# Kernel optimization log

Measured on AMD Instinct MI355X. Metric: run time of the kernel, lower is better.

## Reference

```python
import jax, jax.numpy as jnp
import numpy as np

NEG_SLOPE = 0.01  # F.leaky_relu default
FGW = 0.1         # feature_guidance_weight


def gat_layer(x, src, dst, W, att_l, att_r, heads, out_ch, concat):
    N = x.shape[0]
    # reward-based guidance weights (L1-normalized over nodes, F.normalize p=1 dim=0)
    rw = 1.0 / (jnp.abs(x[:, -1:]) + 1e-6)                    # [N,1]
    rw = rw / jnp.maximum(jnp.sum(jnp.abs(rw), axis=0), 1e-12)
    h = (x @ W).reshape(N, heads, out_ch)                      # [N,H,C]
    # per-node attention halves, gathered per edge (avoids [E,H,C] for scores)
    al = jnp.sum(h * att_l, axis=-1)                           # [N,H] (x_i side)
    ar = jnp.sum(h * att_r, axis=-1)                           # [N,H] (x_j side)
    alpha = jax.nn.leaky_relu(al[dst] + ar[src], NEG_SLOPE)    # [E,H]
    alpha = alpha + FGW * jnp.log(rw[src])                     # guidance from source node
    # segment softmax over incoming edges of each target node (PyG softmax)
    m = jax.ops.segment_max(alpha, dst, num_segments=N)        # [N,H]
    e = jnp.exp(alpha - m[dst])
    s = jax.ops.segment_sum(e, dst, num_segments=N)
    alpha = e / (s[dst] + 1e-16)                               # [E,H]
    # weighted scatter-aggregate of source features
    msg = h[src] * alpha[:, :, None]                           # [E,H,C]
    out = jax.ops.segment_sum(msg, dst, num_segments=N)        # [N,H,C]
    if concat:
        return out.reshape(N, heads * out_ch)
    return out.mean(axis=1)


def setup_inputs() -> dict:
    key = jax.random.key(0)
    ks = jax.random.split(key, 10)
    N, E, D_IN, HID, HEADS, D_OUT = 50000, 800000, 128, 64, 4, 1

    def xavier(k, shape, fan_in, fan_out):
        a = jnp.sqrt(6.0 / (fan_in + fan_out))
        return jax.random.uniform(k, shape, jnp.float32, -a, a)

    x = jax.random.normal(ks[0], (N, D_IN), jnp.float32)
    edge_index = jax.random.randint(ks[1], (2, E), 0, N, jnp.int32)
    W1 = xavier(ks[2], (D_IN, HEADS * HID), D_IN, HEADS * HID)
    att_l1 = xavier(ks[3], (1, HEADS, HID), HID, HID)
    att_r1 = xavier(ks[4], (1, HEADS, HID), HID, HID)
    W2 = xavier(ks[5], (HEADS * HID, HID), HEADS * HID, HID)
    att_l2 = xavier(ks[6], (1, 1, HID), HID, HID)
    att_r2 = xavier(ks[7], (1, 1, HID), HID, HID)
    fc_w = xavier(ks[8], (HID, D_OUT), HID, D_OUT)
    fc_b = jnp.zeros((D_OUT,), jnp.float32)
    return {"x": x, "edge_index": edge_index, "W1": W1, "att_l1": att_l1,
            "att_r1": att_r1, "W2": W2, "att_l2": att_l2, "att_r2": att_r2,
            "fc_w": fc_w, "fc_b": fc_b}


def reference(x, edge_index, W1, att_l1, att_r1, W2, att_l2, att_r2, fc_w, fc_b):
    src, dst = edge_index[0], edge_index[1]
    HID, HEADS = 64, 4
    h = gat_layer(x, src, dst, W1, att_l1, att_r1, HEADS, HID, concat=True)
    h = jax.nn.elu(h)  # dropout omitted (eval mode)
    h = gat_layer(h, src, dst, W2, att_l2, att_r2, 1, HID, concat=False)
    h = jax.nn.elu(h)
    return h @ fc_w + fc_b
```

## Files before the change

kernel.cpp:

```cpp
#include <hip/hip_runtime.h>
#include <hip/hip_bf16.h>

typedef __hip_bfloat16 bf16;
typedef __attribute__((ext_vector_type(8))) short bf16x8;
typedef __attribute__((ext_vector_type(4))) float f32x4;

#define NEG_SLOPE 0.01f
#define FGW 0.1f

__device__ __forceinline__ float b2f(bf16 v) { return __bfloat162float(v); }

__device__ __forceinline__ float ldf(const void* p, size_t i, int isbf) {
    return isbf ? b2f(((const bf16*)p)[i]) : ((const float*)p)[i];
}

__device__ __forceinline__ float bu2f(unsigned short u) {
    return __uint_as_float(((unsigned)u) << 16);
}
__device__ __forceinline__ unsigned short f2bu(float f) {
    return __bfloat16_as_ushort(__float2bfloat16(f));
}

__device__ __forceinline__ float waveReduceSum(float v) {
#pragma unroll
    for (int o = 32; o > 0; o >>= 1) v += __shfl_down(v, o, 64);
    return v;
}

#define ATOMIC_ADD_F32(p, v) unsafeAtomicAdd((p), (v))

__global__ __launch_bounds__(256) void k_degdet(const int* __restrict__ ei, int* __restrict__ deg, int E,
                                                const unsigned short* __restrict__ xr,
                                                float* __restrict__ sscal, int* __restrict__ flag,
                                                const void* __restrict__ W1, const void* __restrict__ W2,
                                                unsigned short* __restrict__ Wp1h,
                                                unsigned short* __restrict__ Wp1l,
                                                unsigned short* __restrict__ Wp2) {
    __shared__ int sflag;
    const int t = threadIdx.x;
    const bool packer = (blockIdx.x < 128);
    if (packer) {
        if (t < 64) {
            int big = 0;
            for (int i = t; i < 256; i += 64) {
                int ex = (xr[i] >> 7) & 0xFF;
                if (ex >= 0xBF) big = 1;
            }
            unsigned long long mk = __ballot(big);
            if (t == 0) sflag = (mk == 0ull) ? 1 : 0;
        }
        __syncthreads();
        const int isbf = sflag;
        if (blockIdx.x == 0 && t == 0) {
            *flag = isbf;
            sscal[0] = 0.f; sscal[1] = 0.f;
        }
        int id = blockIdx.x * 256 + t;
        {
            int j = id & 7, l = (id >> 3) & 63, ko = (id >> 9) & 3, T = id >> 11;
            int k = ko * 32 + (l >> 4) * 8 + j, col = T * 16 + (l & 15);
            float wv = ldf(W1, (size_t)k * 256 + col, isbf);
            unsigned short hi = f2bu(wv);
            Wp1h[id] = hi;
            Wp1l[id] = f2bu(wv - bu2f(hi));
        }
        if (id < 16384) {
            int j = id & 7, l = (id >> 3) & 63, ko = (id >> 9) & 7, T = id >> 12;
            int k = ko * 32 + (l >> 4) * 8 + j, col = T * 16 + (l & 15);
            Wp2[id] = f2bu(ldf(W2, (size_t)k * 64 + col, isbf));
        }
    }
    int e = blockIdx.x * 256 + t;
    if (e < E) atomicAdd(&deg[ei[E + e]], 1);
}

__global__ __launch_bounds__(256) void k_scanA(const int* __restrict__ deg, int* __restrict__ tmp,
                                               int* __restrict__ bsum, int N) {
    __shared__ int part[256];
    const int t = threadIdx.x;
    int i = blockIdx.x * 256 + t;
    int v = (i < N) ? ((deg[i] + 3) & ~3) : 0;
    part[t] = v;
    __syncthreads();
    for (int o = 1; o < 256; o <<= 1) {
        int add = (t >= o) ? part[t - o] : 0;
        __syncthreads();
        part[t] += add;
        __syncthreads();
    }
    if (i < N) tmp[i] = part[t];
    if (t == 255) bsum[blockIdx.x] = part[255];
}

__global__ __launch_bounds__(256) void k_scanB(int* __restrict__ bsum, int nb, int* __restrict__ rowptrN) {
    __shared__ int part[256];
    const int t = threadIdx.x;
    const int K = (nb + 255) / 256;
    int vs[8];
    int lsum = 0;
#pragma unroll
    for (int k = 0; k < 8; k++) {
        int idx = t * K + k;
        vs[k] = (k < K && idx < nb) ? bsum[idx] : 0;
        lsum += vs[k];
    }
    part[t] = lsum;
    __syncthreads();
    for (int o = 1; o < 256; o <<= 1) {
        int add = (t >= o) ? part[t - o] : 0;
        __syncthreads();
        part[t] += add;
        __syncthreads();
    }
    int excl = part[t] - lsum;
#pragma unroll
    for (int k = 0; k < 8; k++) {
        int idx = t * K + k;
        if (k < K && idx < nb) { bsum[idx] = excl; excl += vs[k]; }
    }
    if (t == 255) *rowptrN = part[255];
}

__global__ __launch_bounds__(256) void k_scanC(const int* __restrict__ deg, const int* __restrict__ tmp,
                                               const int* __restrict__ bsum, int* __restrict__ rowptr,
                                               int* __restrict__ cursor, int* __restrict__ csr_src, int N) {
    int i = blockIdx.x * 256 + threadIdx.x;
    if (i >= N) return;
    int dg = deg[i];
    int pd = (dg + 3) & ~3;
    int base = bsum[blockIdx.x] + tmp[i] - pd;
    rowptr[i] = base;
    cursor[i] = 0;
    for (int j = dg; j < pd; j++) csr_src[base + j] = N;
}

__global__ __launch_bounds__(256) void k_scatter(const int* __restrict__ ei, const int* __restrict__ rowptr,
                                                 int* __restrict__ cursor, int* __restrict__ csr_src, int E) {
    int e = blockIdx.x * 256 + threadIdx.x;
    if (e >= E) return;
    int d = ei[E + e];
    int pos = atomicAdd(&cursor[d], 1);
    csr_src[rowptr[d] + pos] = ei[e];
}

__global__ __launch_bounds__(256) void k_gemm1f(const void* __restrict__ x,
                                                const unsigned short* __restrict__ Wp1h,
                                                const unsigned short* __restrict__ Wp1l,
                                                const void* __restrict__ attl,
                                                const void* __restrict__ attr,
                                                unsigned short* __restrict__ h1,
                                                float* __restrict__ pk1,
                                                float* __restrict__ al1,
                                                float* __restrict__ rwS,
                                                int N, const int* __restrict__ flag) {
    const int isbf = *flag;
    __shared__ unsigned short Ash[64 * 136];
    __shared__ unsigned short Asl[64 * 136];
    __shared__ float rpart[64];
    const int row0 = blockIdx.x * 64;
    const int t = threadIdx.x;
    const int w = t >> 6, lane = t & 63;
    const int m = lane & 15, quad = lane >> 4;

    if (blockIdx.x == 0) {
        if (t < 32) *reinterpret_cast<uint4*>(&h1[(size_t)N * 256 + t * 8]) = (uint4){0u, 0u, 0u, 0u};
        if (t < 8) pk1[(size_t)N * 8 + t] = (t < 4) ? -1e30f : 0.f;
    }

#pragma unroll
    for (int it = 0; it < 4; it++) {
        int idx = it * 256 + t;
        int r = idx >> 4, c = idx & 15;
        float v[8];
        if (row0 + r < N) {
            if (isbf) {
                const unsigned short* xu = (const unsigned short*)x;
                uint4 raw = *reinterpret_cast<const uint4*>(xu + (size_t)(row0 + r) * 128 + c * 8);
                const unsigned short* rs = (const unsigned short*)&raw;
#pragma unroll
                for (int k = 0; k < 8; k++) v[k] = bu2f(rs[k]);
            } else {
                const float* xf = (const float*)x;
                float4 a = *reinterpret_cast<const float4*>(xf + (size_t)(row0 + r) * 128 + c * 8);
                float4 b = *reinterpret_cast<const float4*>(xf + (size_t)(row0 + r) * 128 + c * 8 + 4);
                v[0] = a.x; v[1] = a.y; v[2] = a.z; v[3] = a.w;
                v[4] = b.x; v[5] = b.y; v[6] = b.z; v[7] = b.w;
            }
        } else {
#pragma unroll
            for (int k = 0; k < 8; k++) v[k] = 0.f;
        }
        unsigned short hi[8];
#pragma unroll
        for (int k = 0; k < 8; k++) hi[k] = f2bu(v[k]);
        *reinterpret_cast<uint4*>(&Ash[r * 136 + c * 8]) = *reinterpret_cast<const uint4*>(hi);
        if (!isbf) {
            unsigned short lo[8];
#pragma unroll
            for (int k = 0; k < 8; k++) lo[k] = f2bu(v[k] - bu2f(hi[k]));
            *reinterpret_cast<uint4*>(&Asl[r * 136 + c * 8]) = *reinterpret_cast<const uint4*>(lo);
        }
    }
    __syncthreads();

    bf16x8 Bh[4][4];
#pragma unroll
    for (int tt = 0; tt < 4; tt++)
#pragma unroll
        for (int ko = 0; ko < 4; ko++)
            Bh[tt][ko] = *reinterpret_cast<const bf16x8*>(
                &Wp1h[(size_t)(((w * 4 + tt) * 4 + ko) * 64 + lane) * 8]);
    float avl[4], avr[4];
#pragma unroll
    for (int tt = 0; tt < 4; tt++) {
        int col = (w * 4 + tt) * 16 + m;
        avl[tt] = ldf(attl, col, isbf);
        avr[tt] = ldf(attr, col, isbf);
    }
    for (int sub = 0; sub < 4; sub++) {
        const int rbase = sub * 16;
        bf16x8 Ah[4];
#pragma unroll
        for (int ko = 0; ko < 4; ko++)
            Ah[ko] = *reinterpret_cast<const bf16x8*>(&Ash[(rbase + m) * 136 + ko * 32 + quad * 8]);
        f32x4 Cf[4];
#pragma unroll
        for (int tt = 0; tt < 4; tt++) Cf[tt] = (f32x4){0.f, 0.f, 0.f, 0.f};
        if (isbf) {
#pragma unroll
            for (int ko = 0; ko < 4; ko++)
#pragma unroll
                for (int tt = 0; tt < 4; tt++)
                    Cf[tt] = __builtin_amdgcn_mfma_f32_16x16x32_bf16(Ah[ko], Bh[tt][ko], Cf[tt], 0, 0, 0);
        } else {
            bf16x8 Al[4];
#pragma unroll
            for (int ko = 0; ko < 4; ko++)
                Al[ko] = *reinterpret_cast<const bf16x8*>(&Asl[(rbase + m) * 136 + ko * 32 + quad * 8]);
#pragma unroll
            for (int ko = 0; ko < 4; ko++)
#pragma unroll
                for (int tt = 0; tt < 4; tt++) {
                    Cf[tt] = __builtin_amdgcn_mfma_f32_16x16x32_bf16(Ah[ko], Bh[tt][ko], Cf[tt], 0, 0, 0);
                    Cf[tt] = __builtin_amdgcn_mfma_f32_16x16x32_bf16(Al[ko], Bh[tt][ko], Cf[tt], 0, 0, 0);
                    bf16x8 Bl = *reinterpret_cast<const bf16x8*>(
                        &Wp1l[(size_t)(((w * 4 + tt) * 4 + ko) * 64 + lane) * 8]);
                    Cf[tt] = __builtin_amdgcn_mfma_f32_16x16x32_bf16(Ah[ko], Bl, Cf[tt], 0, 0, 0);
                }
        }
#pragma unroll
        for (int tt = 0; tt < 4; tt++) {
            int col = (w * 4 + tt) * 16 + m;
#pragma unroll
            for (int reg = 0; reg < 4; reg++) {
                int row = row0 + rbase + quad * 4 + reg;
                if (row < N) h1[(size_t)row * 256 + col] = f2bu(Cf[tt][reg]);
            }
        }
        if (w == 3 && m == 15) {
#pragma unroll
            for (int reg = 0; reg < 4; reg++) {
                int row = row0 + rbase + quad * 4 + reg;
                if (row < N) pk1[(size_t)row * 8 + 5] = Cf[3][reg];
            }
        }
        float sl[4], sr[4];
#pragma unroll
        for (int reg = 0; reg < 4; reg++) {
            float a = 0.f, b = 0.f;
#pragma unroll
            for (int tt = 0; tt < 4; tt++) {
                a = fmaf(avl[tt], Cf[tt][reg], a);
                b = fmaf(avr[tt], Cf[tt][reg], b);
            }
            sl[reg] = a; sr[reg] = b;
        }
#pragma unroll
        for (int off = 8; off >= 1; off >>= 1) {
#pragma unroll
            for (int reg = 0; reg < 4; reg++) {
                sl[reg] += __shfl_down(sl[reg], off, 64);
                sr[reg] += __shfl_down(sr[reg], off, 64);
            }
        }
        if (m == 0) {
#pragma unroll
            for (int reg = 0; reg < 4; reg++) {
                int row = row0 + rbase + quad * 4 + reg;
                if (row < N) {
                    al1[(size_t)row * 4 + w] = sl[reg];
                    pk1[(size_t)row * 8 + w] = sr[reg];
                }
            }
        }
    }
    if (t < 64) {
        int row = row0 + t;
        float rr = 0.f;
        if (row < N) {
            float a = fabsf(ldf(x, (size_t)row * 128 + 127, isbf));
            rr = 1.f / (a + 1e-6f);
            pk1[(size_t)row * 8 + 4] = logf(rr);
        }
        rpart[t] = rr;
    }
    __syncthreads();
    if (t == 0) {
        float s = 0.f;
#pragma unroll
        for (int i = 0; i < 64; i++) s += rpart[i];
        ATOMIC_ADD_F32(rwS, s);
    }
}

__global__ __launch_bounds__(256) void k_agg1(const int* __restrict__ rowptr,
                                              const int* __restrict__ csr_src,
                                              const float* __restrict__ al1,
                                              const float* __restrict__ pk1,
                                              const float* __restrict__ rwS,
                                              const unsigned short* __restrict__ h1,
                                              unsigned short* __restrict__ x2b,
                                              float* __restrict__ x2c, int N) {
    const int lane = threadIdx.x & 63;
    const int wid = threadIdx.x >> 6;
    const int q = lane & 15;
    const int g = lane >> 4;
    const int h = q >> 2;
    const bool last15 = (q == 15);
    const float gl = FGW * logf(fmaxf(*rwS, 1e-12f));
    const unsigned qo = (unsigned)q * 32u;
    const unsigned ho4 = (unsigned)h * 4u;
    const char* pk1c = (const char*)pk1;
    const char* h1c  = (const char*)h1;
    const int stride = gridDim.x * 4;

    for (int d = blockIdx.x * 4 + wid; d < N; d += stride) {
        const float al_h = al1[(size_t)d * 4 + h];
        const int beg = rowptr[d], end = rowptr[d + 1];

        float acc[16];
#pragma unroll
        for (int k = 0; k < 16; k++) acc[k] = 0.f;
        float ssum = 0.f;

        for (int base = beg; base < end; base += 32) {
            const int nst = min(end - base, 32) >> 2;

            int sj[8];
#pragma unroll
            for (int k = 0; k < 8; k++)
                if (k < nst) sj[k] = csr_src[base + k * 4 + g];

            float arP[4]; float2 lcP[4]; uint4 h0P[4], h1P[4];

#define LD1(K) do {                                                                   \
        int s_ = sj[(K)];                                                             \
        unsigned po_ = (unsigned)s_ * 32u;                                            \
        arP[(K) & 3] = *reinterpret_cast<const float*>(pk1c + po_ + ho4);             \
        lcP[(K) & 3] = *reinterpret_cast<const float2*>(pk1c + po_ + 16u);            \
        unsigned ho_ = (unsigned)s_ * 512u + qo;                                      \
        h0P[(K) & 3] = *reinterpret_cast<const uint4*>(h1c + ho_);                    \
        h1P[(K) & 3] = *reinterpret_cast<const uint4*>(h1c + ho_ + 16u);              \
    } while (0)

#define CONS1(K) do {                                                                 \
        float a_ = al_h + arP[(K) & 3];                                               \
        a_ = fmaxf(a_, NEG_SLOPE * a_);                                               \
        a_ = fmaf(FGW, lcP[(K) & 3].x, a_ - gl);                                      \
        float e_ = __expf(a_);                                                        \
        ssum += e_;                                                                   \
        uint4 cb0_ = h0P[(K) & 3], cb1_ = h1P[(K) & 3];                               \
        unsigned uu_; float lo_, hi_;                                                 \
        uu_ = cb0_.x; lo_ = __uint_as_float(uu_ << 16); hi_ = __uint_as_float(uu_ & 0xFFFF0000u); \
        acc[0] = fmaf(e_, lo_, acc[0]);  acc[1] = fmaf(e_, hi_, acc[1]);              \
        uu_ = cb0_.y; lo_ = __uint_as_float(uu_ << 16); hi_ = __uint_as_float(uu_ & 0xFFFF0000u); \
        acc[2] = fmaf(e_, lo_, acc[2]);  acc[3] = fmaf(e_, hi_, acc[3]);              \
        uu_ = cb0_.z; lo_ = __uint_as_float(uu_ << 16); hi_ = __uint_as_float(uu_ & 0xFFFF0000u); \
        acc[4] = fmaf(e_, lo_, acc[4]);  acc[5] = fmaf(e_, hi_, acc[5]);              \
        uu_ = cb0_.w; lo_ = __uint_as_float(uu_ << 16); hi_ = __uint_as_float(uu_ & 0xFFFF0000u); \
        acc[6] = fmaf(e_, lo_, acc[6]);  acc[7] = fmaf(e_, hi_, acc[7]);              \
        uu_ = cb1_.x; lo_ = __uint_as_float(uu_ << 16); hi_ = __uint_as_float(uu_ & 0xFFFF0000u); \
        acc[8] = fmaf(e_, lo_, acc[8]);  acc[9] = fmaf(e_, hi_, acc[9]);              \
        uu_ = cb1_.y; lo_ = __uint_as_float(uu_ << 16); hi_ = __uint_as_float(uu_ & 0xFFFF0000u); \
        acc[10] = fmaf(e_, lo_, acc[10]); acc[11] = fmaf(e_, hi_, acc[11]);           \
        uu_ = cb1_.z; lo_ = __uint_as_float(uu_ << 16); hi_ = __uint_as_float(uu_ & 0xFFFF0000u); \
        acc[12] = fmaf(e_, lo_, acc[12]); acc[13] = fmaf(e_, hi_, acc[13]);           \
        uu_ = cb1_.w; lo_ = __uint_as_float(uu_ << 16); hi_ = __uint_as_float(uu_ & 0xFFFF0000u); \
        hi_ = last15 ? lcP[(K) & 3].y : hi_;    \
        acc[14] = fmaf(e_, lo_, acc[14]); acc[15] = fmaf(e_, hi_, acc[15]);           \
    } while (0)

            LD1(0);
            if (1 < nst) LD1(1);
            if (2 < nst) LD1(2);
#pragma unroll
            for (int k = 0; k < 8; k++) {
                if (k >= nst) break;
                if (k + 3 < 8) { if (k + 3 < nst) LD1(k + 3); }
                CONS1(k);
            }
#undef LD1
#undef CONS1
        }

#pragma unroll
        for (int k = 0; k < 16; k++) {
            acc[k] += __shfl_xor(acc[k], 16, 64);
            acc[k] += __shfl_xor(acc[k], 32, 64);
        }
        ssum += __shfl_xor(ssum, 16, 64);
        ssum += __shfl_xor(ssum, 32, 64);

        const float inv = 1.f / (ssum + 1e-16f);
        float o0 = (g == 0 ? acc[0] : g == 1 ? acc[4]  : g == 2 ? acc[8]  : acc[12]);
        float o1 = (g == 0 ? acc[1] : g == 1 ? acc[5]  : g == 2 ? acc[9]  : acc[13]);
        float o2 = (g == 0 ? acc[2] : g == 1 ? acc[6]  : g == 2 ? acc[10] : acc[14]);
        float o3 = (g == 0 ? acc[3] : g == 1 ? acc[7]  : g == 2 ? acc[11] : acc[15]);
        o0 *= inv; o1 *= inv; o2 *= inv; o3 *= inv;
        o0 = (o0 > 0.f) ? o0 : expm1f(o0);
        o1 = (o1 > 0.f) ? o1 : expm1f(o1);
        o2 = (o2 > 0.f) ? o2 : expm1f(o2);
        o3 = (o3 > 0.f) ? o3 : expm1f(o3);
        uint2 ob;
        ob.x = (unsigned)f2bu(o0) | ((unsigned)f2bu(o1) << 16);
        ob.y = (unsigned)f2bu(o2) | ((unsigned)f2bu(o3) << 16);
        *reinterpret_cast<uint2*>(&x2b[(size_t)d * 256 + q * 16 + g * 4]) = ob;
        if (lane == 63) x2c[d] = o3;
    }
}

__global__ __launch_bounds__(256) void k_gemm2f(const unsigned short* __restrict__ x2b,
                                                const float* __restrict__ x2c,
                                                const unsigned short* __restrict__ Wp2,
                                                const void* __restrict__ attl,
                                                const void* __restrict__ attr,
                                                unsigned short* __restrict__ h2,
                                                float* __restrict__ pk2,
                                                float* __restrict__ al2,
                                                float* __restrict__ rwS2,
                                                int N, const int* __restrict__ flag) {
    const int isbf = *flag;
    __shared__ unsigned short As[64 * 264];
    __shared__ float pl[4 * 64], pr[4 * 64], rpart[64];
    const int row0 = blockIdx.x * 64;
    const int t = threadIdx.x;
    const int w = t >> 6, lane = t & 63;
    const int m = lane & 15, quad = lane >> 4;

    if (blockIdx.x == 0) {
        if (t < 8) *reinterpret_cast<uint4*>(&h2[(size_t)N * 64 + t * 8]) = (uint4){0u, 0u, 0u, 0u};
        if (t == 0) { pk2[(size_t)N * 2] = -1e30f; pk2[(size_t)N * 2 + 1] = 0.f; }
    }

#pragma unroll
    for (int it = 0; it < 8; it++) {
        int idx = it * 256 + t;
        int r = idx >> 5, c = idx & 31;
        uint4 v = {0u, 0u, 0u, 0u};
        if (row0 + r < N)
            v = *reinterpret_cast<const uint4*>(x2b + (size_t)(row0 + r) * 256 + c * 8);
        *reinterpret_cast<uint4*>(&As[r * 264 + c * 8]) = v;
    }
    __syncthreads();
    bf16x8 Bf[8];
#pragma unroll
    for (int ko = 0; ko < 8; ko++)
        Bf[ko] = *reinterpret_cast<const bf16x8*>(&Wp2[(size_t)((w * 8 + ko) * 64 + lane) * 8]);
    f32x4 Cf[4];
#pragma unroll
    for (int sub = 0; sub < 4; sub++) Cf[sub] = (f32x4){0.f, 0.f, 0.f, 0.f};
#pragma unroll
    for (int ko = 0; ko < 8; ko++)
#pragma unroll
        for (int sub = 0; sub < 4; sub++) {
            bf16x8 Af = *reinterpret_cast<const bf16x8*>(
                &As[(sub * 16 + m) * 264 + ko * 32 + quad * 8]);
            Cf[sub] = __builtin_amdgcn_mfma_f32_16x16x32_bf16(Af, Bf[ko], Cf[sub], 0, 0, 0);
        }
    int col = w * 16 + m;
    float avl = ldf(attl, col, isbf);
    float avr = ldf(attr, col, isbf);
#pragma unroll
    for (int sub = 0; sub < 4; sub++) {
#pragma unroll
        for (int reg = 0; reg < 4; reg++) {
            int row = row0 + sub * 16 + quad * 4 + reg;
            if (row < N) h2[(size_t)row * 64 + col] = f2bu(Cf[sub][reg]);
        }
        float sl[4], sr[4];
#pragma unroll
        for (int reg = 0; reg < 4; reg++) { sl[reg] = avl * Cf[sub][reg]; sr[reg] = avr * Cf[sub][reg]; }
#pragma unroll
        for (int off = 8; off >= 1; off >>= 1) {
#pragma unroll
            for (int reg = 0; reg < 4; reg++) {
                sl[reg] += __shfl_down(sl[reg], off, 64);
                sr[reg] += __shfl_down(sr[reg], off, 64);
            }
        }
        if (m == 0) {
#pragma unroll
            for (int reg = 0; reg < 4; reg++) {
                pl[sub * 64 + w * 16 + quad * 4 + reg] = sl[reg];
                pr[sub * 64 + w * 16 + quad * 4 + reg] = sr[reg];
            }
        }
    }
    __syncthreads();
    if (t < 64) {
        int row = row0 + t;
        int sub = t >> 4, ri = t & 15;
        float rr = 0.f;
        if (row < N) {
            al2[row] = pl[sub * 64 + ri] + pl[sub * 64 + 16 + ri] + pl[sub * 64 + 32 + ri] + pl[sub * 64 + 48 + ri];
            pk2[(size_t)row * 2] = pr[sub * 64 + ri] + pr[sub * 64 + 16 + ri] + pr[sub * 64 + 32 + ri] + pr[sub * 64 + 48 + ri];
            float a = fabsf(x2c[row]);
            rr = 1.f / (a + 1e-6f);
            pk2[(size_t)row * 2 + 1] = logf(rr);
        }
        rpart[t] = rr;
    }
    __syncthreads();
    if (t == 0) {
        float s = 0.f;
#pragma unroll
        for (int i = 0; i < 64; i++) s += rpart[i];
        ATOMIC_ADD_F32(rwS2, s);
    }
}

__global__ __launch_bounds__(256) void k_agg2(const int* __restrict__ rowptr,
                                              const int* __restrict__ csr_src,
                                              const float* __restrict__ al2,
                                              const float* __restrict__ pk2,
                                              const float* __restrict__ rwS2,
                                              const unsigned short* __restrict__ h2,
                                              const void* __restrict__ fcw,
                                              const void* __restrict__ fcb,
                                              void* __restrict__ y, int N,
                                              const int* __restrict__ flag) {
    const int isbf = *flag;
    const int lane = threadIdx.x & 63;
    const int wid = threadIdx.x >> 6;
    const int q = lane & 15;
    const int g = lane >> 4;
    const float gl2 = FGW * logf(fmaxf(*rwS2, 1e-12f));
    const char* pk2c = (const char*)pk2;
    const char* h2c  = (const char*)h2;
    const unsigned qo8 = (unsigned)q * 8u;
    const int stride = gridDim.x * 4;
    const float fw = ldf(fcw, q * 4 + g, isbf);
    const float fb = ldf(fcb, 0, isbf);

    for (int d = blockIdx.x * 4 + wid; d < N; d += stride) {
        const float al_d = al2[d];
        const int beg = rowptr[d], end = rowptr[d + 1];

        float acc[4];
#pragma unroll
        for (int k = 0; k < 4; k++) acc[k] = 0.f;
        float ssum = 0.f;

        for (int base = beg; base < end; base += 32) {
            const int nst = min(end - base, 32) >> 2;

            int sj[8];
#pragma unroll
            for (int k = 0; k < 8; k++)
                if (k < nst) sj[k] = csr_src[base + k * 4 + g];

            float2 pvP[4]; uint2 hbP[4];

#define LD2(K) do {                                                                    \
        int s_ = sj[(K)];                                                              \
        pvP[(K) & 3] = *reinterpret_cast<const float2*>(pk2c + (unsigned)s_ * 8u);     \
        hbP[(K) & 3] = *reinterpret_cast<const uint2*>(h2c + (unsigned)s_ * 128u + qo8); \
    } while (0)

#define CONS2(K) do {                                                                  \
        float a_ = al_d + pvP[(K) & 3].x;                                              \
        a_ = fmaxf(a_, NEG_SLOPE * a_);                                                \
        a_ = fmaf(FGW, pvP[(K) & 3].y, a_ - gl2);                                      \
        float e_ = __expf(a_);                                                         \
        ssum += e_;                                                                    \
        unsigned uu_ = hbP[(K) & 3].x;                                                 \
        acc[0] = fmaf(e_, __uint_as_float(uu_ << 16), acc[0]);                         \
        acc[1] = fmaf(e_, __uint_as_float(uu_ & 0xFFFF0000u), acc[1]);                 \
        uu_ = hbP[(K) & 3].y;                                                          \
        acc[2] = fmaf(e_, __uint_as_float(uu_ << 16), acc[2]);                         \
        acc[3] = fmaf(e_, __uint_as_float(uu_ & 0xFFFF0000u), acc[3]);                 \
    } while (0)

            LD2(0);
            if (1 < nst) LD2(1);
            if (2 < nst) LD2(2);
#pragma unroll
            for (int k = 0; k < 8; k++) {
                if (k >= nst) break;
                if (k + 3 < 8) { if (k + 3 < nst) LD2(k + 3); }
                CONS2(k);
            }
#undef LD2
#undef CONS2
        }

#pragma unroll
        for (int k = 0; k < 4; k++) {
            acc[k] += __shfl_xor(acc[k], 16, 64);
            acc[k] += __shfl_xor(acc[k], 32, 64);
        }
        ssum += __shfl_xor(ssum, 16, 64);
        ssum += __shfl_xor(ssum, 32, 64);

        float v = (g == 0 ? acc[0] : g == 1 ? acc[1] : g == 2 ? acc[2] : acc[3]) / (ssum + 1e-16f);
        v = (v > 0.f) ? v : expm1f(v);
        float r = waveReduceSum(v * fw);
        if (lane == 0) {
            float o = r + fb;
            if (isbf) ((bf16*)y)[d] = __float2bfloat16(o);
            else      ((float*)y)[d] = o;
        }
    }
}

extern "C" void kernel_launch(void* const* d_in, const int* in_sizes, int n_in,
                              void* d_out, int out_size, void* d_ws, size_t ws_size,
                              hipStream_t stream) {
    const void* x     = d_in[0];
    const int*  ei    = (const int*)d_in[1];
    const void* W1    = d_in[2];
    const void* attl1 = d_in[3];
    const void* attr1 = d_in[4];
    const void* W2    = d_in[5];
    const void* attl2 = d_in[6];
    const void* attr2 = d_in[7];
    const void* fcw   = d_in[8];
    const void* fcb   = d_in[9];

    const int N = in_sizes[0] / 128;
    const int E = in_sizes[1] / 2;
    const int NB = (N + 255) / 256;
    const int E2 = E + 4 * N;

    float* p = (float*)d_ws;
    unsigned short* h1 = (unsigned short*)p; p += (size_t)(N + 1) * 128;
    float* pk1    = p; p += (size_t)(N + 1) * 8;
    float* al1    = p; p += (size_t)N * 4;
    unsigned short* x2b = (unsigned short*)p; p += (size_t)N * 128;
    float* x2c    = p; p += (size_t)N;
    float* pk2    = p; p += (size_t)(N + 1) * 2;
    float* al2    = p; p += (size_t)N;
    int* rowptr   = (int*)p; p += (size_t)N + 1;
    int* deg      = (int*)p; p += (size_t)N;
    int* cursor   = (int*)p; p += (size_t)N;
    int* stmp     = (int*)p; p += (size_t)N;
    int* bsum     = (int*)p; p += (size_t)NB;
    int* csr_src  = (int*)p; p += (size_t)E2;
    p = (float*)(((uintptr_t)p + 15) & ~(uintptr_t)15);
    unsigned short* Wp1h = (unsigned short*)p; p += 16384;
    unsigned short* Wp1l = (unsigned short*)p; p += 16384;
    unsigned short* Wp2  = (unsigned short*)p; p += 8192;
    float* sscal  = p; p += 4;
    int* dflag = (int*)(sscal + 2);

    unsigned short* h2 = h1;

    hipMemsetAsync(deg, 0, (size_t)N * 4, stream);

    k_degdet<<<(E + 255) / 256, 256, 0, stream>>>(ei, deg, E, (const unsigned short*)x, sscal, dflag,
                                                  W1, W2, Wp1h, Wp1l, Wp2);
    k_scanA<<<NB, 256, 0, stream>>>(deg, stmp, bsum, N);
    k_scanB<<<1, 256, 0, stream>>>(bsum, NB, &rowptr[N]);
    k_scanC<<<NB, 256, 0, stream>>>(deg, stmp, bsum, rowptr, cursor, csr_src, N);
    k_scatter<<<(E + 255) / 256, 256, 0, stream>>>(ei, rowptr, cursor, csr_src, E);

    const int ag = min((N + 3) / 4, 2048);

    k_gemm1f<<<(N + 63) / 64, 256, 0, stream>>>(x, Wp1h, Wp1l, attl1, attr1, h1, pk1, al1,
                                                &sscal[0], N, dflag);
    k_agg1<<<ag, 256, 0, stream>>>(rowptr, csr_src, al1, pk1,
                                   &sscal[0], h1, x2b, x2c, N);

    k_gemm2f<<<(N + 63) / 64, 256, 0, stream>>>(x2b, x2c, Wp2, attl2, attr2, h2, pk2, al2,
                                                &sscal[1], N, dflag);
    k_agg2<<<ag, 256, 0, stream>>>(rowptr, csr_src, al2, pk2,
                                   &sscal[1], h2, fcw, fcb, d_out, N, dflag);
}
```

Before: 319.6 us.

## Tile aggregation kernels by feature column slice across blocks with per-head packed scores

Replaces the one-wave-per-node aggregation kernels with column-tiled SpMM kernels. Each block handles 32 nodes for one 64-byte feature slice, with 8 nodes per wave and padded edge loops up to the wave's max degree. The intent is better L2 locality: concurrent blocks touch only one column slice of the gathered h rows. A new repack kernel writes per-head (ar, log rw) pairs. Layer 2 writes partial fc dot products to a buffer reduced by a final kernel. The costs are recomputing exp scores in every tile, extra kernel launches, and wasted work on degree imbalance within a wave.

```diff
diff --git a/kernel.cpp b/kernel.cpp
--- a/kernel.cpp
+++ b/kernel.cpp
@@ -19,12 +19,6 @@
 }
 __device__ __forceinline__ unsigned short f2bu(float f) {
     return __bfloat16_as_ushort(__float2bfloat16(f));
-}
-
-__device__ __forceinline__ float waveReduceSum(float v) {
-#pragma unroll
-    for (int o = 32; o > 0; o >>= 1) v += __shfl_down(v, o, 64);
-    return v;
 }
 
 #define ATOMIC_ADD_F32(p, v) unsafeAtomicAdd((p), (v))
@@ -313,119 +307,117 @@
     }
 }
 
-__global__ __launch_bounds__(256) void k_agg1(const int* __restrict__ rowptr,
-                                              const int* __restrict__ csr_src,
-                                              const float* __restrict__ al1,
-                                              const float* __restrict__ pk1,
-                                              const float* __restrict__ rwS,
-                                              const unsigned short* __restrict__ h1,
-                                              unsigned short* __restrict__ x2b,
-                                              float* __restrict__ x2c, int N) {
+__global__ __launch_bounds__(256) void k_pkh(const float* __restrict__ pk1, float* __restrict__ pkh, int N) {
+    int d = blockIdx.x * 256 + threadIdx.x;
+    if (d > N) return;
+    const size_t np1 = (size_t)N + 1;
+    float lr = pk1[(size_t)d * 8 + 4];
+#pragma unroll
+    for (int h = 0; h < 4; h++) {
+        float ar = pk1[(size_t)d * 8 + h];
+        pkh[h * np1 * 2 + (size_t)d * 2]     = ar;
+        pkh[h * np1 * 2 + (size_t)d * 2 + 1] = lr;
+    }
+}
+
+__global__ __launch_bounds__(256) void k_spmm1(const int* __restrict__ rowptr,
+                                               const int* __restrict__ csr_src,
+                                               const float* __restrict__ al1,
+                                               const float* __restrict__ pkh,
+                                               const float* __restrict__ pk1,
+                                               const float* __restrict__ rwS,
+                                               const unsigned short* __restrict__ h1,
+                                               unsigned short* __restrict__ x2b,
+                                               float* __restrict__ x2c, int N) {
+    const int tile = blockIdx.x & 7;
+    const int chunk = blockIdx.x >> 3;
+    const int wid = threadIdx.x >> 6;
     const int lane = threadIdx.x & 63;
-    const int wid = threadIdx.x >> 6;
-    const int q = lane & 15;
-    const int g = lane >> 4;
-    const int h = q >> 2;
-    const bool last15 = (q == 15);
+    const int g = lane >> 3;
+    const int c = lane & 7;
+    const int d = chunk * 32 + wid * 8 + g;
+    const bool vd = d < N;
+    const int hh = tile >> 1;
     const float gl = FGW * logf(fmaxf(*rwS, 1e-12f));
-    const unsigned qo = (unsigned)q * 32u;
-    const unsigned ho4 = (unsigned)h * 4u;
-    const char* pk1c = (const char*)pk1;
-    const char* h1c  = (const char*)h1;
-    const int stride = gridDim.x * 4;
-
-    for (int d = blockIdx.x * 4 + wid; d < N; d += stride) {
-        const float al_h = al1[(size_t)d * 4 + h];
-        const int beg = rowptr[d], end = rowptr[d + 1];
-
-        float acc[16];
-#pragma unroll
-        for (int k = 0; k < 16; k++) acc[k] = 0.f;
-        float ssum = 0.f;
-
-        for (int base = beg; base < end; base += 32) {
-            const int nst = min(end - base, 32) >> 2;
-
-            int sj[8];
-#pragma unroll
-            for (int k = 0; k < 8; k++)
-                if (k < nst) sj[k] = csr_src[base + k * 4 + g];
-
-            float arP[4]; float2 lcP[4]; uint4 h0P[4], h1P[4];
-
-#define LD1(K) do {                                                                   \
-        int s_ = sj[(K)];                                                             \
-        unsigned po_ = (unsigned)s_ * 32u;                                            \
-        arP[(K) & 3] = *reinterpret_cast<const float*>(pk1c + po_ + ho4);             \
-        lcP[(K) & 3] = *reinterpret_cast<const float2*>(pk1c + po_ + 16u);            \
-        unsigned ho_ = (unsigned)s_ * 512u + qo;                                      \
-        h0P[(K) & 3] = *reinterpret_cast<const uint4*>(h1c + ho_);                    \
-        h1P[(K) & 3] = *reinterpret_cast<const uint4*>(h1c + ho_ + 16u);              \
+    const float al_h = vd ? al1[(size_t)d * 4 + hh] : 0.f;
+    const float* php = pkh + (size_t)hh * ((size_t)(N + 1) * 2);
+    const char* h1c = (const char*)h1;
+    const unsigned hoff = (unsigned)tile * 64u + (unsigned)c * 8u;
+    const bool p7 = (tile == 7) && (c == 7);
+
+    int beg = 0, pd = 0;
+    if (vd) { beg = rowptr[d]; pd = rowptr[d + 1] - beg; }
+    int mx = pd;
+    mx = max(mx, __shfl_xor(mx, 8, 64));
+    mx = max(mx, __shfl_xor(mx, 16, 64));
+    mx = max(mx, __shfl_xor(mx, 32, 64));
+
+    float acc0 = 0.f, acc1 = 0.f, acc2 = 0.f, acc3 = 0.f, ssum = 0.f;
+
+    for (int b = 0; b < mx; b += 8) {
+        const int nst = min(mx - b, 8);
+        int sj[8];
+#pragma unroll
+        for (int k = 0; k < 8; k++)
+            if (k < nst) {
+                int j = b + k;
+                int sv = csr_src[beg + ((j < pd) ? j : 0)];
+                sj[k] = (j < pd) ? sv : N;
+            }
+        float2 pvP[4]; uint2 hbP[4]; float cfP[4];
+
+#define LDH(K) do {                                                                    \
+        int s_ = sj[(K)];                                                              \
+        pvP[(K) & 3] = *reinterpret_cast<const float2*>(php + (size_t)s_ * 2);         \
+        hbP[(K) & 3] = *reinterpret_cast<const uint2*>(h1c + (unsigned)s_ * 512u + hoff); \
+        cfP[(K) & 3] = 0.f;                                                            \
+        if (p7) cfP[(K) & 3] = pk1[(size_t)s_ * 8 + 5];                                \
     } while (0)
 
-#define CONS1(K) do {                                                                 \
-        float a_ = al_h + arP[(K) & 3];                                               \
-        a_ = fmaxf(a_, NEG_SLOPE * a_);                                               \
-        a_ = fmaf(FGW, lcP[(K) & 3].x, a_ - gl);                                      \
-        float e_ = __expf(a_);                                                        \
-        ssum += e_;                                                                   \
-        uint4 cb0_ = h0P[(K) & 3], cb1_ = h1P[(K) & 3];                               \
-        unsigned uu_; float lo_, hi_;                                                 \
-        uu_ = cb0_.x; lo_ = __uint_as_float(uu_ << 16); hi_ = __uint_as_float(uu_ & 0xFFFF0000u); \
-        acc[0] = fmaf(e_, lo_, acc[0]);  acc[1] = fmaf(e_, hi_, acc[1]);              \
-        uu_ = cb0_.y; lo_ = __uint_as_float(uu_ << 16); hi_ = __uint_as_float(uu_ & 0xFFFF0000u); \
-        acc[2] = fmaf(e_, lo_, acc[2]);  acc[3] = fmaf(e_, hi_, acc[3]);              \
-        uu_ = cb0_.z; lo_ = __uint_as_float(uu_ << 16); hi_ = __uint_as_float(uu_ & 0xFFFF0000u); \
-        acc[4] = fmaf(e_, lo_, acc[4]);  acc[5] = fmaf(e_, hi_, acc[5]);              \
-        uu_ = cb0_.w; lo_ = __uint_as_float(uu_ << 16); hi_ = __uint_as_float(uu_ & 0xFFFF0000u); \
-        acc[6] = fmaf(e_, lo_, acc[6]);  acc[7] = fmaf(e_, hi_, acc[7]);              \
-        uu_ = cb1_.x; lo_ = __uint_as_float(uu_ << 16); hi_ = __uint_as_float(uu_ & 0xFFFF0000u); \
-        acc[8] = fmaf(e_, lo_, acc[8]);  acc[9] = fmaf(e_, hi_, acc[9]);              \
-        uu_ = cb1_.y; lo_ = __uint_as_float(uu_ << 16); hi_ = __uint_as_float(uu_ & 0xFFFF0000u); \
-        acc[10] = fmaf(e_, lo_, acc[10]); acc[11] = fmaf(e_, hi_, acc[11]);           \
-        uu_ = cb1_.z; lo_ = __uint_as_float(uu_ << 16); hi_ = __uint_as_float(uu_ & 0xFFFF0000u); \
-        acc[12] = fmaf(e_, lo_, acc[12]); acc[13] = fmaf(e_, hi_, acc[13]);           \
-        uu_ = cb1_.w; lo_ = __uint_as_float(uu_ << 16); hi_ = __uint_as_float(uu_ & 0xFFFF0000u); \
-        hi_ = last15 ? lcP[(K) & 3].y : hi_;    \
-        acc[14] = fmaf(e_, lo_, acc[14]); acc[15] = fmaf(e_, hi_, acc[15]);           \
+#define CONSH(K) do {                                                                  \
+        float2 pv_ = pvP[(K) & 3];                                                     \
+        float a_ = al_h + pv_.x;                                                       \
+        a_ = fmaxf(a_, NEG_SLOPE * a_);                                                \
+        a_ = fmaf(FGW, pv_.y, a_ - gl);                                                \
+        float e_ = __expf(a_);                                                         \
+        ssum += e_;                                                                    \
+        uint2 hb_ = hbP[(K) & 3];                                                      \
+        float v0 = __uint_as_float(hb_.x << 16);                                       \
+        float v1 = __uint_as_float(hb_.x & 0xFFFF0000u);                               \
+        float v2 = __uint_as_float(hb_.y << 16);                                       \
+        float v3 = __uint_as_float(hb_.y & 0xFFFF0000u);                               \
+        v3 = p7 ? cfP[(K) & 3] : v3;         \
+        acc0 = fmaf(e_, v0, acc0);                                                     \
+        acc1 = fmaf(e_, v1, acc1);                                                     \
+        acc2 = fmaf(e_, v2, acc2);                                                     \
+        acc3 = fmaf(e_, v3, acc3);                                                     \
     } while (0)
 
-            LD1(0);
-            if (1 < nst) LD1(1);
-            if (2 < nst) LD1(2);
-#pragma unroll
-            for (int k = 0; k < 8; k++) {
-                if (k >= nst) break;
-                if (k + 3 < 8) { if (k + 3 < nst) LD1(k + 3); }
-                CONS1(k);
-            }
-#undef LD1
-#undef CONS1
-        }
-
-#pragma unroll
-        for (int k = 0; k < 16; k++) {
-            acc[k] += __shfl_xor(acc[k], 16, 64);
-            acc[k] += __shfl_xor(acc[k], 32, 64);
-        }
-        ssum += __shfl_xor(ssum, 16, 64);
-        ssum += __shfl_xor(ssum, 32, 64);
-
-        const float inv = 1.f / (ssum + 1e-16f);
-        float o0 = (g == 0 ? acc[0] : g == 1 ? acc[4]  : g == 2 ? acc[8]  : acc[12]);
-        float o1 = (g == 0 ? acc[1] : g == 1 ? acc[5]  : g == 2 ? acc[9]  : acc[13]);
-        float o2 = (g == 0 ? acc[2] : g == 1 ? acc[6]  : g == 2 ? acc[10] : acc[14]);
-        float o3 = (g == 0 ? acc[3] : g == 1 ? acc[7]  : g == 2 ? acc[11] : acc[15]);
-        o0 *= inv; o1 *= inv; o2 *= inv; o3 *= inv;
-        o0 = (o0 > 0.f) ? o0 : expm1f(o0);
-        o1 = (o1 > 0.f) ? o1 : expm1f(o1);
-        o2 = (o2 > 0.f) ? o2 : expm1f(o2);
-        o3 = (o3 > 0.f) ? o3 : expm1f(o3);
+        LDH(0);
+        if (1 < nst) LDH(1);
+        if (2 < nst) LDH(2);
+#pragma unroll
+        for (int k = 0; k < 8; k++) {
+            if (k >= nst) break;
+            if (k + 3 < 8) { if (k + 3 < nst) LDH(k + 3); }
+            CONSH(k);
+        }
+#undef LDH
+#undef CONSH
+    }
+
+    const float inv = 1.f / (ssum + 1e-16f);
+    float o0 = acc0 * inv, o1 = acc1 * inv, o2 = acc2 * inv, o3 = acc3 * inv;
+    o0 = (o0 > 0.f) ? o0 : expm1f(o0);
+    o1 = (o1 > 0.f) ? o1 : expm1f(o1);
+    o2 = (o2 > 0.f) ? o2 : expm1f(o2);
+    o3 = (o3 > 0.f) ? o3 : expm1f(o3);
+    if (vd) {
         uint2 ob;
         ob.x = (unsigned)f2bu(o0) | ((unsigned)f2bu(o1) << 16);
         ob.y = (unsigned)f2bu(o2) | ((unsigned)f2bu(o3) << 16);
-        *reinterpret_cast<uint2*>(&x2b[(size_t)d * 256 + q * 16 + g * 4]) = ob;
-        if (lane == 63) x2c[d] = o3;
+        *reinterpret_cast<uint2*>(&x2b[(size_t)d * 256 + tile * 32 + c * 4]) = ob;
+        if (p7) x2c[d] = o3;
     }
 }
 
@@ -529,98 +521,108 @@
     }
 }
 
-__global__ __launch_bounds__(256) void k_agg2(const int* __restrict__ rowptr,
-                                              const int* __restrict__ csr_src,
-                                              const float* __restrict__ al2,
-                                              const float* __restrict__ pk2,
-                                              const float* __restrict__ rwS2,
-                                              const unsigned short* __restrict__ h2,
-                                              const void* __restrict__ fcw,
-                                              const void* __restrict__ fcb,
-                                              void* __restrict__ y, int N,
-                                              const int* __restrict__ flag) {
+__global__ __launch_bounds__(256) void k_spmm2(const int* __restrict__ rowptr,
+                                               const int* __restrict__ csr_src,
+                                               const float* __restrict__ al2,
+                                               const float* __restrict__ pk2,
+                                               const float* __restrict__ rwS2,
+                                               const unsigned short* __restrict__ h2,
+                                               const void* __restrict__ fcw,
+                                               float* __restrict__ yf, int N,
+                                               const int* __restrict__ flag) {
     const int isbf = *flag;
+    const int tile = blockIdx.x & 1;
+    const int chunk = blockIdx.x >> 1;
+    const int wid = threadIdx.x >> 6;
     const int lane = threadIdx.x & 63;
-    const int wid = threadIdx.x >> 6;
-    const int q = lane & 15;
-    const int g = lane >> 4;
+    const int g = lane >> 3;
+    const int c = lane & 7;
+    const int d = chunk * 32 + wid * 8 + g;
+    const bool vd = d < N;
     const float gl2 = FGW * logf(fmaxf(*rwS2, 1e-12f));
-    const char* pk2c = (const char*)pk2;
-    const char* h2c  = (const char*)h2;
-    const unsigned qo8 = (unsigned)q * 8u;
-    const int stride = gridDim.x * 4;
-    const float fw = ldf(fcw, q * 4 + g, isbf);
-    const float fb = ldf(fcb, 0, isbf);
-
-    for (int d = blockIdx.x * 4 + wid; d < N; d += stride) {
-        const float al_d = al2[d];
-        const int beg = rowptr[d], end = rowptr[d + 1];
-
-        float acc[4];
-#pragma unroll
-        for (int k = 0; k < 4; k++) acc[k] = 0.f;
-        float ssum = 0.f;
-
-        for (int base = beg; base < end; base += 32) {
-            const int nst = min(end - base, 32) >> 2;
-
-            int sj[8];
-#pragma unroll
-            for (int k = 0; k < 8; k++)
-                if (k < nst) sj[k] = csr_src[base + k * 4 + g];
-
-            float2 pvP[4]; uint2 hbP[4];
-
-#define LD2(K) do {                                                                    \
+    const float al_d = vd ? al2[d] : 0.f;
+    const char* h2c = (const char*)h2;
+    const unsigned hoff = (unsigned)tile * 64u + (unsigned)c * 8u;
+    float fw0 = ldf(fcw, tile * 32 + c * 4 + 0, isbf);
+    float fw1 = ldf(fcw, tile * 32 + c * 4 + 1, isbf);
+    float fw2 = ldf(fcw, tile * 32 + c * 4 + 2, isbf);
+    float fw3 = ldf(fcw, tile * 32 + c * 4 + 3, isbf);
+
+    int beg = 0, pd = 0;
+    if (vd) { beg = rowptr[d]; pd = rowptr[d + 1] - beg; }
+    int mx = pd;
+    mx = max(mx, __shfl_xor(mx, 8, 64));
+    mx = max(mx, __shfl_xor(mx, 16, 64));
+    mx = max(mx, __shfl_xor(mx, 32, 64));
+
+    float acc0 = 0.f, acc1 = 0.f, acc2 = 0.f, acc3 = 0.f, ssum = 0.f;
+
+    for (int b = 0; b < mx; b += 8) {
+        const int nst = min(mx - b, 8);
+        int sj[8];
+#pragma unroll
+        for (int k = 0; k < 8; k++)
+            if (k < nst) {
+                int j = b + k;
+                int sv = csr_src[beg + ((j < pd) ? j : 0)];
+                sj[k] = (j < pd) ? sv : N;
+            }
+        float2 pvP[4]; uint2 hbP[4];
+
+#define LDH2(K) do {                                                                   \
         int s_ = sj[(K)];                                                              \
-        pvP[(K) & 3] = *reinterpret_cast<const float2*>(pk2c + (unsigned)s_ * 8u);     \
-        hbP[(K) & 3] = *reinterpret_cast<const uint2*>(h2c + (unsigned)s_ * 128u + qo8); \
+        pvP[(K) & 3] = *reinterpret_cast<const float2*>(pk2 + (size_t)s_ * 2);         \
+        hbP[(K) & 3] = *reinterpret_cast<const uint2*>(h2c + (unsigned)s_ * 128u + hoff); \
     } while (0)
 
-#define CONS2(K) do {                                                                  \
-        float a_ = al_d + pvP[(K) & 3].x;                                              \
+#define CONSH2(K) do {                                                                 \
+        float2 pv_ = pvP[(K) & 3];                                                     \
+        float a_ = al_d + pv_.x;                                                       \
         a_ = fmaxf(a_, NEG_SLOPE * a_);                                                \
-        a_ = fmaf(FGW, pvP[(K) & 3].y, a_ - gl2);                                      \
+        a_ = fmaf(FGW, pv_.y, a_ - gl2);                                               \
         float e_ = __expf(a_);                                                         \
         ssum += e_;                                                                    \
-        unsigned uu_ = hbP[(K) & 3].x;                                                 \
-        acc[0] = fmaf(e_, __uint_as_float(uu_ << 16), acc[0]);                         \
-        acc[1] = fmaf(e_, __uint_as_float(uu_ & 0xFFFF0000u), acc[1]);                 \
-        uu_ = hbP[(K) & 3].y;                                                          \
-        acc[2] = fmaf(e_, __uint_as_float(uu_ << 16), acc[2]);                         \
-        acc[3] = fmaf(e_, __uint_as_float(uu_ & 0xFFFF0000u), acc[3]);                 \
+        uint2 hb_ = hbP[(K) & 3];                                                      \
+        acc0 = fmaf(e_, __uint_as_float(hb_.x << 16), acc0);                           \
+        acc1 = fmaf(e_, __uint_as_float(hb_.x & 0xFFFF0000u), acc1);                   \
+        acc2 = fmaf(e_, __uint_as_float(hb_.y << 16), acc2);                           \
+        acc3 = fmaf(e_, __uint_as_float(hb_.y & 0xFFFF0000u), acc3);                   \
     } while (0)
 
-            LD2(0);
-            if (1 < nst) LD2(1);
-            if (2 < nst) LD2(2);
-#pragma unroll
-            for (int k = 0; k < 8; k++) {
-                if (k >= nst) break;
-                if (k + 3 < 8) { if (k + 3 < nst) LD2(k + 3); }
-                CONS2(k);
-            }
-#undef LD2
-#undef CONS2
-        }
-
-#pragma unroll
-        for (int k = 0; k < 4; k++) {
-            acc[k] += __shfl_xor(acc[k], 16, 64);
-            acc[k] += __shfl_xor(acc[k], 32, 64);
-        }
-        ssum += __shfl_xor(ssum, 16, 64);
-        ssum += __shfl_xor(ssum, 32, 64);
-
-        float v = (g == 0 ? acc[0] : g == 1 ? acc[1] : g == 2 ? acc[2] : acc[3]) / (ssum + 1e-16f);
-        v = (v > 0.f) ? v : expm1f(v);
-        float r = waveReduceSum(v * fw);
-        if (lane == 0) {
-            float o = r + fb;
-            if (isbf) ((bf16*)y)[d] = __float2bfloat16(o);
-            else      ((float*)y)[d] = o;
-        }
-    }
+        LDH2(0);
+        if (1 < nst) LDH2(1);
+        if (2 < nst) LDH2(2);
+#pragma unroll
+        for (int k = 0; k < 8; k++) {
+            if (k >= nst) break;
+            if (k + 3 < 8) { if (k + 3 < nst) LDH2(k + 3); }
+            CONSH2(k);
+        }
+#undef LDH2
+#undef CONSH2
+    }
+
+    const float inv = 1.f / (ssum + 1e-16f);
+    float o0 = acc0 * inv, o1 = acc1 * inv, o2 = acc2 * inv, o3 = acc3 * inv;
+    o0 = (o0 > 0.f) ? o0 : expm1f(o0);
+    o1 = (o1 > 0.f) ? o1 : expm1f(o1);
+    o2 = (o2 > 0.f) ? o2 : expm1f(o2);
+    o3 = (o3 > 0.f) ? o3 : expm1f(o3);
+    float part = fmaf(o0, fw0, fmaf(o1, fw1, fmaf(o2, fw2, o3 * fw3)));
+    part += __shfl_xor(part, 1, 64);
+    part += __shfl_xor(part, 2, 64);
+    part += __shfl_xor(part, 4, 64);
+    if (vd && c == 0) yf[(size_t)tile * N + d] = part;
+}
+
+__global__ __launch_bounds__(256) void k_fin(const float* __restrict__ yf, const void* __restrict__ fcb,
+                                             void* __restrict__ y, int N, const int* __restrict__ flag) {
+    int d = blockIdx.x * 256 + threadIdx.x;
+    if (d >= N) return;
+    const int isbf = *flag;
+    float o = yf[d] + yf[(size_t)N + d] + ldf(fcb, 0, isbf);
+    if (isbf) ((bf16*)y)[d] = __float2bfloat16(o);
+    else      ((float*)y)[d] = o;
 }
 
 extern "C" void kernel_launch(void* const* d_in, const int* in_sizes, int n_in,
@@ -645,11 +647,13 @@
     float* p = (float*)d_ws;
     unsigned short* h1 = (unsigned short*)p; p += (size_t)(N + 1) * 128;
     float* pk1    = p; p += (size_t)(N + 1) * 8;
+    float* pkh    = p; p += (size_t)(N + 1) * 8;
     float* al1    = p; p += (size_t)N * 4;
     unsigned short* x2b = (unsigned short*)p; p += (size_t)N * 128;
     float* x2c    = p; p += (size_t)N;
     float* pk2    = p; p += (size_t)(N + 1) * 2;
     float* al2    = p; p += (size_t)N;
+    float* yf     = p; p += (size_t)N * 2;
     int* rowptr   = (int*)p; p += (size_t)N + 1;
     int* deg      = (int*)p; p += (size_t)N;
     int* cursor   = (int*)p; p += (size_t)N;
@@ -674,15 +678,17 @@
     k_scanC<<<NB, 256, 0, stream>>>(deg, stmp, bsum, rowptr, cursor, csr_src, N);
     k_scatter<<<(E + 255) / 256, 256, 0, stream>>>(ei, rowptr, cursor, csr_src, E);
 
-    const int ag = min((N + 3) / 4, 2048);
+    const int NCH = (N + 31) / 32;
 
     k_gemm1f<<<(N + 63) / 64, 256, 0, stream>>>(x, Wp1h, Wp1l, attl1, attr1, h1, pk1, al1,
                                                 &sscal[0], N, dflag);
-    k_agg1<<<ag, 256, 0, stream>>>(rowptr, csr_src, al1, pk1,
-                                   &sscal[0], h1, x2b, x2c, N);
+    k_pkh<<<(N + 256) / 256, 256, 0, stream>>>(pk1, pkh, N);
+    k_spmm1<<<8 * NCH, 256, 0, stream>>>(rowptr, csr_src, al1, pkh, pk1,
+                                         &sscal[0], h1, x2b, x2c, N);
 
     k_gemm2f<<<(N + 63) / 64, 256, 0, stream>>>(x2b, x2c, Wp2, attl2, attr2, h2, pk2, al2,
                                                 &sscal[1], N, dflag);
-    k_agg2<<<ag, 256, 0, stream>>>(rowptr, csr_src, al2, pk2,
-                                   &sscal[1], h2, fcw, fcb, d_out, N, dflag);
-}
+    k_spmm2<<<2 * NCH, 256, 0, stream>>>(rowptr, csr_src, al2, pk2,
+                                         &sscal[1], h2, fcw, yf, N, dflag);
+    k_fin<<<(N + 255) / 256, 256, 0, stream>>>(yf, fcb, d_out, N, dflag);
+}
```

Result: slower. 418.5 us (+31.0%).
